# Kernel tuning notes

Hardware: AMD Instinct MI355X
Metric: run time of the kernel (lower is better)

Reference implementation:

```python
import jax, jax.numpy as jnp
import numpy as np

B, E, O, T = 128, 256, 256, 32
H, P = 768, 256
TEMP = 0.07


def _encode(x, W1, b1, W2, b2):
    # two-layer MLP with ReLU, then L2 normalize (F.normalize, dim=-1)
    h = jax.nn.relu(x @ W1 + b1)
    z = h @ W2 + b2
    n = jnp.maximum(jnp.linalg.norm(z, axis=-1, keepdims=True), 1e-12)
    return z / n


def setup_inputs() -> dict:
    key = jax.random.key(0)
    ks = jax.random.split(key, 11)
    s1 = 1.0 / np.sqrt(H).astype(np.float32)
    s2 = 1.0 / np.sqrt(H).astype(np.float32)
    return {
        "entity_reprs": jax.random.normal(ks[0], (B, E, H), dtype=jnp.float32),
        "opinion_reprs": jax.random.normal(ks[1], (B, O, H), dtype=jnp.float32),
        "positive_pairs": jax.random.randint(ks[2], (B, T, 2), 0, E),
        "eW1": jax.random.normal(ks[3], (H, H), dtype=jnp.float32) * s1,
        "eb1": jnp.zeros((H,), dtype=jnp.float32),
        "eW2": jax.random.normal(ks[4], (H, P), dtype=jnp.float32) * s2,
        "eb2": jnp.zeros((P,), dtype=jnp.float32),
        "oW1": jax.random.normal(ks[5], (H, H), dtype=jnp.float32) * s1,
        "ob1": jnp.zeros((H,), dtype=jnp.float32),
        "oW2": jax.random.normal(ks[6], (H, P), dtype=jnp.float32) * s2,
        "ob2": jnp.zeros((P,), dtype=jnp.float32),
    }


def reference(entity_reprs, opinion_reprs, positive_pairs,
              eW1, eb1, eW2, eb2, oW1, ob1, oW2, ob2):
    # project and normalize (vectorized over batch, unlike the torch loop)
    ep = _encode(entity_reprs, eW1, eb1, eW2, eb2)    # [B,E,P]
    op = _encode(opinion_reprs, oW1, ob1, oW2, ob2)   # [B,O,P]
    sim = jnp.einsum('bep,bop->beo', ep, op) / TEMP   # [B,E,O]

    e_idx = positive_pairs[..., 0]                    # [B,T]
    o_idx = positive_pairs[..., 1]                    # [B,T]
    # gather the similarity row for each positive pair's entity
    rows = jnp.take_along_axis(sim, e_idx[:, :, None], axis=1)          # [B,T,O]
    pos = jnp.take_along_axis(rows, o_idx[:, :, None], axis=2)[..., 0]  # [B,T]
    lse = jax.nn.logsumexp(rows, axis=-1)                               # [B,T]
    # InfoNCE: mean over all pairs of -(pos - logsumexp(row))
    return jnp.mean(lse - pos)
```

## Files before the change

kernel.cpp:

```cpp
#include <hip/hip_runtime.h>
#include <hip/hip_bf16.h>
#include <math.h>

typedef short bf16x8 __attribute__((ext_vector_type(8)));
typedef float f32x4 __attribute__((ext_vector_type(4)));
typedef unsigned short u16;
typedef unsigned int u32;

#define BATCH 128
#define NE 256
#define NO 256
#define NT 32
#define NH 768
#define NP 256
#define NKT 12
#define INV_TEMP 14.285714285714285714f

__device__ __forceinline__ u16 f2bf(float f) {
    union { float f; u32 u; } v; v.f = f;
    u32 u = v.u;
    u += 0x7fffu + ((u >> 16) & 1u);
    return (u16)(u >> 16);
}

__device__ __forceinline__ void gload16(const void* g, void* l) {
    __builtin_amdgcn_global_load_lds(
        (const __attribute__((address_space(1))) unsigned int*)g,
        (__attribute__((address_space(3))) unsigned int*)l,
        16, 0, 0);
}

__device__ __forceinline__ bf16x8 ldfrag(const char* base, int row, int kb, int rs) {
    return *(const bf16x8*)(base + row * 128 + (kb ^ rs));
}

#define PH_SYNC_IN()                                          \
    __builtin_amdgcn_s_barrier();                             \
    asm volatile("s_waitcnt lgkmcnt(0)" ::: "memory");        \
    __builtin_amdgcn_sched_barrier(0);                        \
    __builtin_amdgcn_s_setprio(1);

#define PH_SYNC_OUT()                                         \
    __builtin_amdgcn_s_setprio(0);                            \
    __builtin_amdgcn_s_barrier();

#define PREP_ACONV_OP_BLOCKS   12288
#define PREP_ACONV_EN_BLOCKS   1536
#define PREP_WT1_TILES         576
#define PREP_WT2_TILES         192
#define PREP_TOTAL (PREP_ACONV_OP_BLOCKS + PREP_ACONV_EN_BLOCKS + 2*PREP_WT1_TILES + 2*PREP_WT2_TILES)

__device__ __forceinline__ void aconv_body(const float* __restrict__ A,
                                           const int* __restrict__ pairs,
                                           u16* __restrict__ out, int gid) {
    int row = gid / (NH / 8);
    int q = gid - row * (NH / 8);
    size_t srow;
    if (pairs) {
        int e = pairs[2 * row];
        int b = row >> 5;
        srow = (size_t)(b * NE + e);
    } else {
        srow = (size_t)row;
    }
    const float* p = A + srow * NH + q * 8;
    float4 a0 = *(const float4*)(p);
    float4 a1 = *(const float4*)(p + 4);
    u16 ua[8];
    ua[0] = f2bf(a0.x); ua[1] = f2bf(a0.y); ua[2] = f2bf(a0.z); ua[3] = f2bf(a0.w);
    ua[4] = f2bf(a1.x); ua[5] = f2bf(a1.y); ua[6] = f2bf(a1.z); ua[7] = f2bf(a1.w);
    *(uint4*)(out + (size_t)row * NH + q * 8) = *(uint4*)ua;
}

__global__ __launch_bounds__(256) void prep_kernel(
        const float* __restrict__ opi, const float* __restrict__ ent,
        const int* __restrict__ prs,
        const float* __restrict__ oW1, const float* __restrict__ eW1,
        const float* __restrict__ oW2, const float* __restrict__ eW2,
        u16* __restrict__ A_op, u16* __restrict__ A_en,
        u16* __restrict__ oW1T, u16* __restrict__ eW1T,
        u16* __restrict__ oW2T, u16* __restrict__ eW2T) {
    __shared__ float ttile[32][33];
    const int bid = blockIdx.x;
    const int tid = threadIdx.x;
    if (bid < PREP_ACONV_OP_BLOCKS) {
        aconv_body(opi, nullptr, A_op, bid * 256 + tid);
        return;
    }
    if (bid < PREP_ACONV_OP_BLOCKS + PREP_ACONV_EN_BLOCKS) {
        aconv_body(ent, prs, A_en, (bid - PREP_ACONV_OP_BLOCKS) * 256 + tid);
        return;
    }
    int tb = bid - (PREP_ACONV_OP_BLOCKS + PREP_ACONV_EN_BLOCKS);
    const float* W; u16* WT; int N;
    if (tb < PREP_WT1_TILES)                     { W = oW1; WT = oW1T; N = NH; }
    else if ((tb -= PREP_WT1_TILES) < PREP_WT1_TILES) { W = eW1; WT = eW1T; N = NH; }
    else if ((tb -= PREP_WT1_TILES) < PREP_WT2_TILES) { W = oW2; WT = oW2T; N = NP; }
    else { tb -= PREP_WT2_TILES;                   W = eW2; WT = eW2T; N = NP; }
    const int nk = NH / 32;
    const int tn = tb / nk, tk = tb - tn * nk;
    const int k0 = tk * 32, n0 = tn * 32;
    const int tx = tid & 31, ty = tid >> 5;
    #pragma unroll
    for (int i = 0; i < 4; ++i)
        ttile[ty + 8 * i][tx] = W[(size_t)(k0 + ty + 8 * i) * N + n0 + tx];
    __syncthreads();
    #pragma unroll
    for (int i = 0; i < 4; ++i)
        WT[(size_t)(n0 + ty + 8 * i) * NH + k0 + tx] = f2bf(ttile[tx][ty + 8 * i]);
}

#define G1_STAGE_A(t_, d_)                                                       \
  { _Pragma("unroll")                                                            \
    for (int i_ = 0; i_ < 4; ++i_)                                               \
      gload16((const char*)(ag + (size_t)(i_ * 32 + srow) * NH + (t_) * 64) + sswz, \
              (char*)&As[d_][0] + i_ * 4096 + tid * 16); }
#define G1_STAGE_B(t_, d_)                                                       \
  { _Pragma("unroll")                                                            \
    for (int i_ = 0; i_ < 4; ++i_)                                               \
      gload16((const char*)(bg + (size_t)(i_ * 32 + srow) * NH + (t_) * 64) + sswz, \
              (char*)&Bs[d_][0] + i_ * 4096 + tid * 16); }

__launch_bounds__(256, 2)
__global__ void gemm1_kernel(const u16* __restrict__ A_op, const u16* __restrict__ A_en,
                             const u16* __restrict__ oW1T, const u16* __restrict__ eW1T,
                             const float* __restrict__ ob1, const float* __restrict__ eb1,
                             u16* __restrict__ Hop, u16* __restrict__ Hen) {
    __shared__ u16 As[2][128 * 64];
    __shared__ u16 Bs[2][128 * 64];
    const int cpx = gridDim.x >> 3;
    const int wg = (blockIdx.x & 7) * cpx + (blockIdx.x >> 3);
    const bool isent = wg >= 1536;
    const int wgl = isent ? wg - 1536 : wg;
    const int mt = wgl / 6;
    const int nt = wgl - mt * 6;
    const u16* WT = isent ? eW1T : oW1T;
    const float* bias = isent ? eb1 : ob1;
    u16* outH = isent ? Hen : Hop;
    const u16* Abase = isent ? A_en : A_op;

    const int tid = threadIdx.x;
    const int lane = tid & 63;
    const int w = tid >> 6;
    const int wm = w >> 1, wn = w & 1;
    const int lr = lane & 15;
    const int kq = (lane >> 4) << 4;
    const int rs = (lr & 7) << 4;

    const int srow = tid >> 3;
    const int sswz = ((tid & 7) * 16) ^ ((srow & 7) << 4);
    const u16* ag = Abase + (size_t)(mt * 128) * NH;
    const u16* bg = WT + (size_t)(nt * 128) * NH;

    f32x4 acc[4][4] = {};

    G1_STAGE_A(0, 0);
    G1_STAGE_B(0, 0);
    asm volatile("s_waitcnt vmcnt(0)" ::: "memory");
    __builtin_amdgcn_s_barrier();

    for (int t = 0; t < NKT; ++t) {
        const int d = t & 1;
        const char* Ab = (const char*)&As[d][0];
        const char* Bb = (const char*)&Bs[d][0];
        bf16x8 aF[4], bF[4];
        #pragma unroll
        for (int mf = 0; mf < 4; ++mf) aF[mf] = ldfrag(Ab, wm * 64 + mf * 16 + lr, kq, rs);
        #pragma unroll
        for (int nf = 0; nf < 4; ++nf) bF[nf] = ldfrag(Bb, wn * 64 + nf * 16 + lr, kq, rs);
        if (t < NKT - 1) { G1_STAGE_A(t + 1, d ^ 1); G1_STAGE_B(t + 1, d ^ 1); }
        PH_SYNC_IN();
        #pragma unroll
        for (int mf = 0; mf < 4; ++mf)
            #pragma unroll
            for (int nf = 0; nf < 4; ++nf)
                acc[mf][nf] = __builtin_amdgcn_mfma_f32_16x16x32_bf16(aF[mf], bF[nf], acc[mf][nf], 0, 0, 0);
        PH_SYNC_OUT();
        #pragma unroll
        for (int mf = 0; mf < 4; ++mf) aF[mf] = ldfrag(Ab, wm * 64 + mf * 16 + lr, 64 + kq, rs);
        #pragma unroll
        for (int nf = 0; nf < 4; ++nf) bF[nf] = ldfrag(Bb, wn * 64 + nf * 16 + lr, 64 + kq, rs);
        PH_SYNC_IN();
        #pragma unroll
        for (int mf = 0; mf < 4; ++mf)
            #pragma unroll
            for (int nf = 0; nf < 4; ++nf)
                acc[mf][nf] = __builtin_amdgcn_mfma_f32_16x16x32_bf16(aF[mf], bF[nf], acc[mf][nf], 0, 0, 0);
        __builtin_amdgcn_s_setprio(0);
        asm volatile("s_waitcnt vmcnt(0)" ::: "memory");
        __builtin_amdgcn_sched_barrier(0);
        __builtin_amdgcn_s_barrier();
    }

    const int r0 = (lane >> 4) << 2;
    float bv[4];
    #pragma unroll
    for (int nf = 0; nf < 4; ++nf) bv[nf] = bias[nt * 128 + wn * 64 + nf * 16 + lr];
    #pragma unroll
    for (int mf = 0; mf < 4; ++mf) {
        #pragma unroll
        for (int r = 0; r < 4; ++r) {
            const int row = mt * 128 + wm * 64 + mf * 16 + r0 + r;
            u16* orow = outH + (size_t)row * NH + nt * 128 + wn * 64 + lr;
            #pragma unroll
            for (int nf = 0; nf < 4; ++nf) {
                float v = acc[mf][nf][r] + bv[nf];
                orow[nf * 16] = f2bf(fmaxf(v, 0.0f));
            }
        }
    }
}

#define G2_STAGE_A(t_, d_)                                                       \
  { _Pragma("unroll")                                                            \
    for (int i_ = 0; i_ < 2; ++i_)                                               \
      gload16((const char*)(ag + (size_t)(i_ * 32 + srow) * NH + (t_) * 64) + sswz, \
              (char*)&As2[d_][0] + i_ * 4096 + tid * 16); }
#define G2_STAGE_B(t_, d_)                                                       \
  { _Pragma("unroll")                                                            \
    for (int i_ = 0; i_ < 8; ++i_)                                               \
      gload16((const char*)(WT + (size_t)(i_ * 32 + srow) * NH + (t_) * 64) + sswz, \
              (char*)&Bs2[d_][0] + i_ * 4096 + tid * 16); }

__launch_bounds__(256, 2)
__global__ void gemm2norm_kernel(const u16* __restrict__ Hop, const u16* __restrict__ Hen,
                                 const u16* __restrict__ oW2T, const u16* __restrict__ eW2T,
                                 const float* __restrict__ ob2, const float* __restrict__ eb2,
                                 u16* __restrict__ opn, u16* __restrict__ eps) {
    __shared__ u16 As2[2][64 * 64];
    __shared__ u16 Bs2[2][256 * 64];
    float* nsum = (float*)&As2[0][0];
    const int cpx = gridDim.x >> 3;
    const int wg = (blockIdx.x & 7) * cpx + (blockIdx.x >> 3);
    const bool isent = wg >= 512;
    const int mt = isent ? wg - 512 : wg;
    const u16* Hin = isent ? Hen : Hop;
    const u16* WT = isent ? eW2T : oW2T;
    const float* bias = isent ? eb2 : ob2;
    u16* outZ = isent ? eps : opn;

    const int tid = threadIdx.x;
    const int lane = tid & 63;
    const int wn = tid >> 6;
    const int lr = lane & 15;
    const int kq = (lane >> 4) << 4;
    const int rs = (lr & 7) << 4;

    const int srow = tid >> 3;
    const int sswz = ((tid & 7) * 16) ^ ((srow & 7) << 4);
    const u16* ag = Hin + (size_t)(mt * 64) * NH;

    f32x4 acc[4][4] = {};

    G2_STAGE_A(0, 0);
    G2_STAGE_B(0, 0);
    asm volatile("s_waitcnt vmcnt(0)" ::: "memory");
    __builtin_amdgcn_s_barrier();

    for (int t = 0; t < NKT; ++t) {
        const int d = t & 1;
        const char* Ab = (const char*)&As2[d][0];
        const char* Bb = (const char*)&Bs2[d][0];
        bf16x8 aF[4], bF[4];
        #pragma unroll
        for (int mf = 0; mf < 4; ++mf) aF[mf] = ldfrag(Ab, mf * 16 + lr, kq, rs);
        #pragma unroll
        for (int nf = 0; nf < 4; ++nf) bF[nf] = ldfrag(Bb, wn * 64 + nf * 16 + lr, kq, rs);
        if (t < NKT - 1) { G2_STAGE_A(t + 1, d ^ 1); G2_STAGE_B(t + 1, d ^ 1); }
        PH_SYNC_IN();
        #pragma unroll
        for (int mf = 0; mf < 4; ++mf)
            #pragma unroll
            for (int nf = 0; nf < 4; ++nf)
                acc[mf][nf] = __builtin_amdgcn_mfma_f32_16x16x32_bf16(aF[mf], bF[nf], acc[mf][nf], 0, 0, 0);
        PH_SYNC_OUT();
        #pragma unroll
        for (int mf = 0; mf < 4; ++mf) aF[mf] = ldfrag(Ab, mf * 16 + lr, 64 + kq, rs);
        #pragma unroll
        for (int nf = 0; nf < 4; ++nf) bF[nf] = ldfrag(Bb, wn * 64 + nf * 16 + lr, 64 + kq, rs);
        PH_SYNC_IN();
        #pragma unroll
        for (int mf = 0; mf < 4; ++mf)
            #pragma unroll
            for (int nf = 0; nf < 4; ++nf)
                acc[mf][nf] = __builtin_amdgcn_mfma_f32_16x16x32_bf16(aF[mf], bF[nf], acc[mf][nf], 0, 0, 0);
        __builtin_amdgcn_s_setprio(0);
        asm volatile("s_waitcnt vmcnt(0)" ::: "memory");
        __builtin_amdgcn_sched_barrier(0);
        __builtin_amdgcn_s_barrier();
    }

    const int cc = wn * 64 + lr;
    #pragma unroll
    for (int nf = 0; nf < 4; ++nf) {
        const float bvv = bias[cc + nf * 16];
        #pragma unroll
        for (int mf = 0; mf < 4; ++mf)
            #pragma unroll
            for (int r = 0; r < 4; ++r)
                acc[mf][nf][r] += bvv;
    }
    float rsq[4][4];
    #pragma unroll
    for (int mf = 0; mf < 4; ++mf)
        #pragma unroll
        for (int r = 0; r < 4; ++r) {
            float s = 0.f;
            #pragma unroll
            for (int nf = 0; nf < 4; ++nf) s += acc[mf][nf][r] * acc[mf][nf][r];
            rsq[mf][r] = s;
        }
    #pragma unroll
    for (int mask = 1; mask <= 8; mask <<= 1)
        #pragma unroll
        for (int mf = 0; mf < 4; ++mf)
            #pragma unroll
            for (int r = 0; r < 4; ++r)
                rsq[mf][r] += __shfl_xor(rsq[mf][r], mask);
    const int r0 = (lane >> 4) << 2;
    __syncthreads();
    if (lr == 0) {
        #pragma unroll
        for (int mf = 0; mf < 4; ++mf)
            #pragma unroll
            for (int r = 0; r < 4; ++r)
                nsum[wn * 64 + mf * 16 + r0 + r] = rsq[mf][r];
    }
    __syncthreads();
    #pragma unroll
    for (int mf = 0; mf < 4; ++mf) {
        #pragma unroll
        for (int r = 0; r < 4; ++r) {
            const int row = mf * 16 + r0 + r;
            const float tot = nsum[row] + nsum[64 + row] + nsum[128 + row] + nsum[192 + row];
            const float inv = 1.0f / fmaxf(sqrtf(tot), 1e-12f);
            u16* orow = outZ + (size_t)(mt * 64 + row) * NP + cc;
            #pragma unroll
            for (int nf = 0; nf < 4; ++nf)
                orow[nf * 16] = f2bf(acc[mf][nf][r] * inv);
        }
    }
}

__launch_bounds__(256)
__global__ void score_kernel(const u16* __restrict__ epsel, const u16* __restrict__ opn,
                             const int* __restrict__ pairs, float* __restrict__ partials) {
    __shared__ u16 Asx[16][264];
    __shared__ float simbuf[16][257];
    __shared__ float red[16];
    const int b = blockIdx.x >> 1;
    const int half = blockIdx.x & 1;
    const int rbase = half * 16;
    const int tid = threadIdx.x;
    const int lane = tid & 63;
    const int w = tid >> 6;
    {
        const int row = tid >> 4, q = tid & 15;
        const u16* p = epsel + ((size_t)(b * NT + rbase + row)) * NP + q * 16;
        *(uint4*)&Asx[row][q * 16 + 0] = *(const uint4*)(p + 0);
        *(uint4*)&Asx[row][q * 16 + 8] = *(const uint4*)(p + 8);
    }
    __syncthreads();
    f32x4 acc[4] = {};
    const u16* opb = opn + (size_t)b * NO * NP;
    const int kq = (lane >> 4) << 3;
    for (int kk = 0; kk < NP; kk += 32) {
        bf16x8 af = *(const bf16x8*)&Asx[lane & 15][kk + kq];
        #pragma unroll
        for (int n = 0; n < 4; ++n) {
            bf16x8 bfr = *(const bf16x8*)(opb + (size_t)(w * 64 + n * 16 + (lane & 15)) * NP + kk + kq);
            acc[n] = __builtin_amdgcn_mfma_f32_16x16x32_bf16(af, bfr, acc[n], 0, 0, 0);
        }
    }
    const int r0 = (lane >> 4) << 2;
    #pragma unroll
    for (int n = 0; n < 4; ++n)
        #pragma unroll
        for (int r = 0; r < 4; ++r)
            simbuf[r0 + r][w * 64 + n * 16 + (lane & 15)] = acc[n][r] * INV_TEMP;
    __syncthreads();
    {
        const int row = tid >> 4, sub = tid & 15;
        float s = 0.f;
        #pragma unroll 4
        for (int j = sub; j < NO; j += 16) s += __expf(simbuf[row][j]);
        s += __shfl_xor(s, 1);
        s += __shfl_xor(s, 2);
        s += __shfl_xor(s, 4);
        s += __shfl_xor(s, 8);
        if (sub == 0) {
            const int o = pairs[(b * NT + rbase + row) * 2 + 1];
            red[row] = logf(s) - simbuf[row][o];
        }
    }
    __syncthreads();
    if (tid == 0) {
        float s = 0.f;
        #pragma unroll
        for (int t = 0; t < 16; ++t) s += red[t];
        partials[blockIdx.x] = s;
    }
}

__global__ void reduce_kernel(const float* __restrict__ partials, float* __restrict__ out) {
    const int tid = threadIdx.x;
    float v = partials[tid];
    #pragma unroll
    for (int m = 1; m <= 32; m <<= 1) v += __shfl_xor(v, m);
    __shared__ float s[4];
    if ((tid & 63) == 0) s[tid >> 6] = v;
    __syncthreads();
    if (tid == 0) out[0] = (s[0] + s[1] + s[2] + s[3]) / (float)(BATCH * NT);
}

extern "C" void kernel_launch(void* const* d_in, const int* in_sizes, int n_in,
                              void* d_out, int out_size, void* d_ws, size_t ws_size,
                              hipStream_t stream) {
    const float* ent  = (const float*)d_in[0];
    const float* opi  = (const float*)d_in[1];
    const int*   prs  = (const int*)d_in[2];
    const float* eW1  = (const float*)d_in[3];
    const float* eb1  = (const float*)d_in[4];
    const float* eW2  = (const float*)d_in[5];
    const float* eb2  = (const float*)d_in[6];
    const float* oW1  = (const float*)d_in[7];
    const float* ob1  = (const float*)d_in[8];
    const float* oW2  = (const float*)d_in[9];
    const float* ob2  = (const float*)d_in[10];
    float* out = (float*)d_out;

    char* ws = (char*)d_ws;
    size_t off = 0;
    auto alloc = [&](size_t bytes) {
        void* p = ws + off;
        off += (bytes + 255) & ~(size_t)255;
        return p;
    };
    u16* oW1T = (u16*)alloc((size_t)NH * NH * 2);
    u16* eW1T = (u16*)alloc((size_t)NH * NH * 2);
    u16* oW2T = (u16*)alloc((size_t)NP * NH * 2);
    u16* eW2T = (u16*)alloc((size_t)NP * NH * 2);
    u16* A_op = (u16*)alloc((size_t)BATCH * NO * NH * 2);
    u16* A_en = (u16*)alloc((size_t)BATCH * NT * NH * 2);
    u16* h_op = (u16*)alloc((size_t)BATCH * NO * NH * 2);
    u16* h_en = (u16*)alloc((size_t)BATCH * NT * NH * 2);
    u16* op_n = (u16*)alloc((size_t)BATCH * NO * NP * 2);
    u16* ep_s = (u16*)alloc((size_t)BATCH * NT * NP * 2);
    float* partials = (float*)alloc(2 * BATCH * sizeof(float));
    (void)ws_size; (void)in_sizes; (void)n_in; (void)out_size;

    prep_kernel<<<PREP_TOTAL, 256, 0, stream>>>(opi, ent, prs, oW1, eW1, oW2, eW2,
                                                A_op, A_en, oW1T, eW1T, oW2T, eW2T);

    gemm1_kernel<<<1728, 256, 0, stream>>>(A_op, A_en, oW1T, eW1T, ob1, eb1, h_op, h_en);

    gemm2norm_kernel<<<576, 256, 0, stream>>>(h_op, h_en, oW2T, eW2T, ob2, eb2, op_n, ep_s);

    score_kernel<<<2 * BATCH, 256, 0, stream>>>(ep_s, op_n, prs, partials);
    reduce_kernel<<<1, 256, 0, stream>>>(partials, out);
}
```

Before: 127.1 us.

## Fuse fp32-to-bf16 activation conversion and entity gather into GEMM1 A-tile loads

Removes the separate prep pass that converted opinion/entity activations to bf16 and gathered entity rows into a workspace buffer. GEMM1 now reads fp32 activations directly (with the pair-index gather for entities), converts them in registers, and writes swizzled bf16 into LDS, overlapped with the MFMA phases. This removes a full write-then-reread of the bf16 A matrices through global memory. In exchange each of the six N-tile blocks re-reads the fp32 A rows (twice the bytes of bf16), uses more registers for the staged float4s, and adds VALU conversion work inside the main loop.

After: 174.2 us. +37.1%, slower.

```diff
diff --git a/kernel.cpp b/kernel.cpp
--- a/kernel.cpp
+++ b/kernel.cpp
@@ -44,54 +44,18 @@
     __builtin_amdgcn_s_setprio(0);                            \
     __builtin_amdgcn_s_barrier();
 
-#define PREP_ACONV_OP_BLOCKS   12288
-#define PREP_ACONV_EN_BLOCKS   1536
 #define PREP_WT1_TILES         576
 #define PREP_WT2_TILES         192
-#define PREP_TOTAL (PREP_ACONV_OP_BLOCKS + PREP_ACONV_EN_BLOCKS + 2*PREP_WT1_TILES + 2*PREP_WT2_TILES)
-
-__device__ __forceinline__ void aconv_body(const float* __restrict__ A,
-                                           const int* __restrict__ pairs,
-                                           u16* __restrict__ out, int gid) {
-    int row = gid / (NH / 8);
-    int q = gid - row * (NH / 8);
-    size_t srow;
-    if (pairs) {
-        int e = pairs[2 * row];
-        int b = row >> 5;
-        srow = (size_t)(b * NE + e);
-    } else {
-        srow = (size_t)row;
-    }
-    const float* p = A + srow * NH + q * 8;
-    float4 a0 = *(const float4*)(p);
-    float4 a1 = *(const float4*)(p + 4);
-    u16 ua[8];
-    ua[0] = f2bf(a0.x); ua[1] = f2bf(a0.y); ua[2] = f2bf(a0.z); ua[3] = f2bf(a0.w);
-    ua[4] = f2bf(a1.x); ua[5] = f2bf(a1.y); ua[6] = f2bf(a1.z); ua[7] = f2bf(a1.w);
-    *(uint4*)(out + (size_t)row * NH + q * 8) = *(uint4*)ua;
-}
+#define PREP_TOTAL (2*PREP_WT1_TILES + 2*PREP_WT2_TILES)
 
 __global__ __launch_bounds__(256) void prep_kernel(
-        const float* __restrict__ opi, const float* __restrict__ ent,
-        const int* __restrict__ prs,
         const float* __restrict__ oW1, const float* __restrict__ eW1,
         const float* __restrict__ oW2, const float* __restrict__ eW2,
-        u16* __restrict__ A_op, u16* __restrict__ A_en,
         u16* __restrict__ oW1T, u16* __restrict__ eW1T,
         u16* __restrict__ oW2T, u16* __restrict__ eW2T) {
     __shared__ float ttile[32][33];
-    const int bid = blockIdx.x;
+    int tb = blockIdx.x;
     const int tid = threadIdx.x;
-    if (bid < PREP_ACONV_OP_BLOCKS) {
-        aconv_body(opi, nullptr, A_op, bid * 256 + tid);
-        return;
-    }
-    if (bid < PREP_ACONV_OP_BLOCKS + PREP_ACONV_EN_BLOCKS) {
-        aconv_body(ent, prs, A_en, (bid - PREP_ACONV_OP_BLOCKS) * 256 + tid);
-        return;
-    }
-    int tb = bid - (PREP_ACONV_OP_BLOCKS + PREP_ACONV_EN_BLOCKS);
     const float* W; u16* WT; int N;
     if (tb < PREP_WT1_TILES)                     { W = oW1; WT = oW1T; N = NH; }
     else if ((tb -= PREP_WT1_TILES) < PREP_WT1_TILES) { W = eW1; WT = eW1T; N = NH; }
@@ -110,11 +74,21 @@
         WT[(size_t)(n0 + ty + 8 * i) * NH + k0 + tx] = f2bf(ttile[tx][ty + 8 * i]);
 }
 
-#define G1_STAGE_A(t_, d_)                                                       \
+#define G1_ISSUE_A(t_)                                                           \
   { _Pragma("unroll")                                                            \
-    for (int i_ = 0; i_ < 4; ++i_)                                               \
-      gload16((const char*)(ag + (size_t)(i_ * 32 + srow) * NH + (t_) * 64) + sswz, \
-              (char*)&As[d_][0] + i_ * 4096 + tid * 16); }
+    for (int j_ = 0; j_ < 8; ++j_)                                               \
+      av[j_] = *(const float4*)(ag + (t_) * 64 + j_ * 4); }
+#define G1_WRITE_A(d_)                                                           \
+  { _Pragma("unroll")                                                            \
+    for (int c_ = 0; c_ < 4; ++c_) {                                             \
+      u16 tb_[8];                                                                \
+      tb_[0] = f2bf(av[2*c_].x);   tb_[1] = f2bf(av[2*c_].y);                    \
+      tb_[2] = f2bf(av[2*c_].z);   tb_[3] = f2bf(av[2*c_].w);                    \
+      tb_[4] = f2bf(av[2*c_+1].x); tb_[5] = f2bf(av[2*c_+1].y);                  \
+      tb_[6] = f2bf(av[2*c_+1].z); tb_[7] = f2bf(av[2*c_+1].w);                  \
+      *(uint4*)((char*)&As[d_][0] + arow * 128 +                                 \
+                ((ahalf * 64 + c_ * 16) ^ ((arow & 7) << 4))) = *(uint4*)tb_;    \
+    } }
 #define G1_STAGE_B(t_, d_)                                                       \
   { _Pragma("unroll")                                                            \
     for (int i_ = 0; i_ < 4; ++i_)                                               \
@@ -122,7 +96,8 @@
               (char*)&Bs[d_][0] + i_ * 4096 + tid * 16); }
 
 __launch_bounds__(256, 2)
-__global__ void gemm1_kernel(const u16* __restrict__ A_op, const u16* __restrict__ A_en,
+__global__ void gemm1_kernel(const float* __restrict__ opi, const float* __restrict__ ent,
+                             const int* __restrict__ pairs,
                              const u16* __restrict__ oW1T, const u16* __restrict__ eW1T,
                              const float* __restrict__ ob1, const float* __restrict__ eb1,
                              u16* __restrict__ Hop, u16* __restrict__ Hen) {
@@ -137,7 +112,6 @@
     const u16* WT = isent ? eW1T : oW1T;
     const float* bias = isent ? eb1 : ob1;
     u16* outH = isent ? Hen : Hop;
-    const u16* Abase = isent ? A_en : A_op;
 
     const int tid = threadIdx.x;
     const int lane = tid & 63;
@@ -149,14 +123,25 @@
 
     const int srow = tid >> 3;
     const int sswz = ((tid & 7) * 16) ^ ((srow & 7) << 4);
-    const u16* ag = Abase + (size_t)(mt * 128) * NH;
     const u16* bg = WT + (size_t)(nt * 128) * NH;
 
+    const int arow = tid >> 1;
+    const int ahalf = tid & 1;
+    size_t asrc;
+    {
+        const int prow = mt * 128 + arow;
+        if (isent) asrc = (size_t)((prow >> 5) * NE + pairs[2 * prow]);
+        else       asrc = (size_t)prow;
+    }
+    const float* ag = (isent ? ent : opi) + asrc * NH + ahalf * 32;
+
     f32x4 acc[4][4] = {};
-
-    G1_STAGE_A(0, 0);
+    float4 av[8];
+
+    G1_ISSUE_A(0);
     G1_STAGE_B(0, 0);
-    asm volatile("s_waitcnt vmcnt(0)" ::: "memory");
+    G1_WRITE_A(0);
+    asm volatile("s_waitcnt vmcnt(0) lgkmcnt(0)" ::: "memory");
     __builtin_amdgcn_s_barrier();
 
     for (int t = 0; t < NKT; ++t) {
@@ -168,7 +153,7 @@
         for (int mf = 0; mf < 4; ++mf) aF[mf] = ldfrag(Ab, wm * 64 + mf * 16 + lr, kq, rs);
         #pragma unroll
         for (int nf = 0; nf < 4; ++nf) bF[nf] = ldfrag(Bb, wn * 64 + nf * 16 + lr, kq, rs);
-        if (t < NKT - 1) { G1_STAGE_A(t + 1, d ^ 1); G1_STAGE_B(t + 1, d ^ 1); }
+        if (t < NKT - 1) { G1_ISSUE_A(t + 1); G1_STAGE_B(t + 1, d ^ 1); }
         PH_SYNC_IN();
         #pragma unroll
         for (int mf = 0; mf < 4; ++mf)
@@ -180,6 +165,7 @@
         for (int mf = 0; mf < 4; ++mf) aF[mf] = ldfrag(Ab, wm * 64 + mf * 16 + lr, 64 + kq, rs);
         #pragma unroll
         for (int nf = 0; nf < 4; ++nf) bF[nf] = ldfrag(Bb, wn * 64 + nf * 16 + lr, 64 + kq, rs);
+        if (t < NKT - 1) { G1_WRITE_A(d ^ 1); }
         PH_SYNC_IN();
         #pragma unroll
         for (int mf = 0; mf < 4; ++mf)
@@ -440,8 +426,6 @@
     u16* eW1T = (u16*)alloc((size_t)NH * NH * 2);
     u16* oW2T = (u16*)alloc((size_t)NP * NH * 2);
     u16* eW2T = (u16*)alloc((size_t)NP * NH * 2);
-    u16* A_op = (u16*)alloc((size_t)BATCH * NO * NH * 2);
-    u16* A_en = (u16*)alloc((size_t)BATCH * NT * NH * 2);
     u16* h_op = (u16*)alloc((size_t)BATCH * NO * NH * 2);
     u16* h_en = (u16*)alloc((size_t)BATCH * NT * NH * 2);
     u16* op_n = (u16*)alloc((size_t)BATCH * NO * NP * 2);
@@ -449,10 +433,10 @@
     float* partials = (float*)alloc(2 * BATCH * sizeof(float));
     (void)ws_size; (void)in_sizes; (void)n_in; (void)out_size;
 
-    prep_kernel<<<PREP_TOTAL, 256, 0, stream>>>(opi, ent, prs, oW1, eW1, oW2, eW2,
-                                                A_op, A_en, oW1T, eW1T, oW2T, eW2T);
-
-    gemm1_kernel<<<1728, 256, 0, stream>>>(A_op, A_en, oW1T, eW1T, ob1, eb1, h_op, h_en);
+    prep_kernel<<<PREP_TOTAL, 256, 0, stream>>>(oW1, eW1, oW2, eW2,
+                                                oW1T, eW1T, oW2T, eW2T);
+
+    gemm1_kernel<<<1728, 256, 0, stream>>>(opi, ent, prs, oW1T, eW1T, ob1, eb1, h_op, h_en);
 
     gemm2norm_kernel<<<576, 256, 0, stream>>>(h_op, h_en, oW2T, eW2T, ob2, eb2, op_n, ep_s);
 
```

## Load GEMM1 A operand directly from global into registers, bypassing LDS

Applied to the files above, without the earlier changes.

The A tile for the first GEMM is now prefetched straight from global memory into per-lane MFMA fragment registers, double-buffered across K tiles, instead of being staged through shared memory. Only the weight (B) tile still goes through LDS. This removes the LDS writes and reads for A and halves the kernel's LDS footprint. In exchange it adds VGPR pressure from two register buffers and uses less coalesced global loads, since each pair of wm waves now reads the same A rows redundantly.

After: 174.8 us. 37.5% more time.

```diff
diff --git a/kernel.cpp b/kernel.cpp
--- a/kernel.cpp
+++ b/kernel.cpp
@@ -110,23 +110,55 @@
         WT[(size_t)(n0 + ty + 8 * i) * NH + k0 + tx] = f2bf(ttile[tx][ty + 8 * i]);
 }
 
-#define G1_STAGE_A(t_, d_)                                                       \
-  { _Pragma("unroll")                                                            \
-    for (int i_ = 0; i_ < 4; ++i_)                                               \
-      gload16((const char*)(ag + (size_t)(i_ * 32 + srow) * NH + (t_) * 64) + sswz, \
-              (char*)&As[d_][0] + i_ * 4096 + tid * 16); }
 #define G1_STAGE_B(t_, d_)                                                       \
   { _Pragma("unroll")                                                            \
     for (int i_ = 0; i_ < 4; ++i_)                                               \
       gload16((const char*)(bg + (size_t)(i_ * 32 + srow) * NH + (t_) * 64) + sswz, \
               (char*)&Bs[d_][0] + i_ * 4096 + tid * 16); }
 
+#define G1_PREF_A(dst_, t_)                                                      \
+  { _Pragma("unroll")                                                            \
+    for (int mf_ = 0; mf_ < 4; ++mf_)                                            \
+      _Pragma("unroll")                                                          \
+      for (int ks_ = 0; ks_ < 2; ++ks_)                                          \
+        dst_[mf_][ks_] = *(const bf16x8*)(aLane + (size_t)mf_ * 16 * NH +        \
+                                          (t_) * 64 + ks_ * 32); }
+
+#define G1_TILE(t_, AC_, AN_, d_)                                                \
+  {                                                                              \
+    const char* Bb = (const char*)&Bs[d_][0];                                    \
+    bf16x8 bF[4];                                                                \
+                 \
+    _Pragma("unroll")                                                            \
+    for (int nf = 0; nf < 4; ++nf) bF[nf] = ldfrag(Bb, wn * 64 + nf * 16 + lr, kq, rs); \
+    if ((t_) < NKT - 1) { G1_PREF_A(AN_, (t_) + 1); G1_STAGE_B((t_) + 1, (d_) ^ 1); } \
+    PH_SYNC_IN();                                                                \
+    _Pragma("unroll")                                                            \
+    for (int mf = 0; mf < 4; ++mf)                                               \
+        _Pragma("unroll")                                                        \
+        for (int nf = 0; nf < 4; ++nf)                                           \
+            acc[mf][nf] = __builtin_amdgcn_mfma_f32_16x16x32_bf16(AC_[mf][0], bF[nf], acc[mf][nf], 0, 0, 0); \
+    PH_SYNC_OUT();                                                               \
+                  \
+    _Pragma("unroll")                                                            \
+    for (int nf = 0; nf < 4; ++nf) bF[nf] = ldfrag(Bb, wn * 64 + nf * 16 + lr, 64 + kq, rs); \
+    PH_SYNC_IN();                                                                \
+    _Pragma("unroll")                                                            \
+    for (int mf = 0; mf < 4; ++mf)                                               \
+        _Pragma("unroll")                                                        \
+        for (int nf = 0; nf < 4; ++nf)                                           \
+            acc[mf][nf] = __builtin_amdgcn_mfma_f32_16x16x32_bf16(AC_[mf][1], bF[nf], acc[mf][nf], 0, 0, 0); \
+    __builtin_amdgcn_s_setprio(0);                                               \
+    asm volatile("s_waitcnt vmcnt(0)" ::: "memory");                             \
+    __builtin_amdgcn_sched_barrier(0);                                           \
+    __builtin_amdgcn_s_barrier();                                                \
+  }
+
 __launch_bounds__(256, 2)
 __global__ void gemm1_kernel(const u16* __restrict__ A_op, const u16* __restrict__ A_en,
                              const u16* __restrict__ oW1T, const u16* __restrict__ eW1T,
                              const float* __restrict__ ob1, const float* __restrict__ eb1,
                              u16* __restrict__ Hop, u16* __restrict__ Hen) {
-    __shared__ u16 As[2][128 * 64];
     __shared__ u16 Bs[2][128 * 64];
     const int cpx = gridDim.x >> 3;
     const int wg = (blockIdx.x & 7) * cpx + (blockIdx.x >> 3);
@@ -149,47 +181,21 @@
 
     const int srow = tid >> 3;
     const int sswz = ((tid & 7) * 16) ^ ((srow & 7) << 4);
-    const u16* ag = Abase + (size_t)(mt * 128) * NH;
     const u16* bg = WT + (size_t)(nt * 128) * NH;
+    const u16* aLane = Abase + (size_t)(mt * 128 + wm * 64 + lr) * NH + ((lane >> 4) << 3);
 
     f32x4 acc[4][4] = {};
-
-    G1_STAGE_A(0, 0);
+    bf16x8 aC[4][2], aN[4][2];
+
+    G1_PREF_A(aC, 0);
     G1_STAGE_B(0, 0);
     asm volatile("s_waitcnt vmcnt(0)" ::: "memory");
     __builtin_amdgcn_s_barrier();
 
-    for (int t = 0; t < NKT; ++t) {
-        const int d = t & 1;
-        const char* Ab = (const char*)&As[d][0];
-        const char* Bb = (const char*)&Bs[d][0];
-        bf16x8 aF[4], bF[4];
-        #pragma unroll
-        for (int mf = 0; mf < 4; ++mf) aF[mf] = ldfrag(Ab, wm * 64 + mf * 16 + lr, kq, rs);
-        #pragma unroll
-        for (int nf = 0; nf < 4; ++nf) bF[nf] = ldfrag(Bb, wn * 64 + nf * 16 + lr, kq, rs);
-        if (t < NKT - 1) { G1_STAGE_A(t + 1, d ^ 1); G1_STAGE_B(t + 1, d ^ 1); }
-        PH_SYNC_IN();
-        #pragma unroll
-        for (int mf = 0; mf < 4; ++mf)
-            #pragma unroll
-            for (int nf = 0; nf < 4; ++nf)
-                acc[mf][nf] = __builtin_amdgcn_mfma_f32_16x16x32_bf16(aF[mf], bF[nf], acc[mf][nf], 0, 0, 0);
-        PH_SYNC_OUT();
-        #pragma unroll
-        for (int mf = 0; mf < 4; ++mf) aF[mf] = ldfrag(Ab, wm * 64 + mf * 16 + lr, 64 + kq, rs);
-        #pragma unroll
-        for (int nf = 0; nf < 4; ++nf) bF[nf] = ldfrag(Bb, wn * 64 + nf * 16 + lr, 64 + kq, rs);
-        PH_SYNC_IN();
-        #pragma unroll
-        for (int mf = 0; mf < 4; ++mf)
-            #pragma unroll
-            for (int nf = 0; nf < 4; ++nf)
-                acc[mf][nf] = __builtin_amdgcn_mfma_f32_16x16x32_bf16(aF[mf], bF[nf], acc[mf][nf], 0, 0, 0);
-        __builtin_amdgcn_s_setprio(0);
-        asm volatile("s_waitcnt vmcnt(0)" ::: "memory");
-        __builtin_amdgcn_sched_barrier(0);
-        __builtin_amdgcn_s_barrier();
+    #pragma unroll
+    for (int tt = 0; tt < NKT; tt += 2) {
+        G1_TILE(tt, aC, aN, 0);
+        G1_TILE(tt + 1, aN, aC, 1);
     }
 
     const int r0 = (lane >> 4) << 2;
```
